# Kernel optimization log

Measured on AMD Instinct MI355X. Metric: run time of the kernel, lower is better.

The kernel has to match this reference:

```python
import jax, jax.numpy as jnp
import numpy as np

N1, N2, N3, N4, D = 50000, 100000, 200000, 300000, 256


def setup_inputs() -> dict:
    key = jax.random.key(0)
    ks = jax.random.split(key, 10)
    feat = jax.random.normal(ks[0], (N1, D), dtype=jnp.float32) * 0.5  # scaled so level-4 products stay bounded
    c2a = jax.random.randint(ks[1], (N2,), 0, N1)
    c2b = jax.random.randint(ks[2], (N2,), 0, N1)
    c3a = jax.random.randint(ks[3], (N3,), 0, N2)
    c3b = jax.random.randint(ks[4], (N3,), 0, N2)
    c4a = jax.random.randint(ks[5], (N4,), 0, N3)
    c4b = jax.random.randint(ks[6], (N4,), 0, N3)
    W = jax.random.normal(ks[7], (D, D), dtype=jnp.float32) / jnp.sqrt(jnp.float32(D))
    b = jax.random.normal(ks[8], (D,), dtype=jnp.float32) * 0.01
    return {"feat": feat, "c2a": c2a, "c2b": c2b, "c3a": c3a, "c3b": c3b,
            "c4a": c4a, "c4b": c4b, "W": W, "b": b}


def _scatter_sum(h_parent, ca, cb, num_children):
    # each parent sends its feature to both children; children sum incoming messages
    z = jnp.zeros((num_children, h_parent.shape[1]), dtype=h_parent.dtype)
    return z.at[ca].add(h_parent).at[cb].add(h_parent)


def reference(feat, c2a, c2b, c3a, c3b, c4a, c4b, W, b):
    # upward: prod reduction over the two constituent subpaths (mailbox prod, dim=1)
    h1 = feat
    h2 = h1[c2a] * h1[c2b]            # [N2, D]
    h3 = h2[c3a] * h2[c3b]            # [N3, D]
    h4 = h3[c4a] * h3[c4b]            # [N4, D]
    # downward: sum-scatter parent -> children, h = h + h_down
    h3 = h3 + _scatter_sum(h4, c4a, c4b, h3.shape[0])
    h2 = h2 + _scatter_sum(h3, c3a, c3b, h2.shape[0])
    h1 = h1 + _scatter_sum(h2, c2a, c2b, h1.shape[0])
    # apply_nodes on n1: Linear + SiLU
    out = jax.nn.silu(h1 @ W + b)
    return out
```

## Files before the change

kernel.cpp:

```cpp
#include <hip/hip_runtime.h>
#include <cstdint>
#include <cstddef>

#define DD 256
#define SCAN_BLK 256
#define SCAN_ELEMS 2048

__device__ __forceinline__ float4 ldrow(const float* __restrict__ base, int row, int lane) {
    return ((const float4*)(base + (size_t)row * DD))[lane];
}
__device__ __forceinline__ float4 mul4(float4 a, float4 b) {
    return make_float4(a.x * b.x, a.y * b.y, a.z * b.z, a.w * b.w);
}
__device__ __forceinline__ float4 add4(float4 a, float4 b) {
    return make_float4(a.x + b.x, a.y + b.y, a.z + b.z, a.w + b.w);
}

__global__ void k_count_pairs(const int* __restrict__ ea, const int* __restrict__ eb,
                              int ne, int* __restrict__ cnt) {
    int e = blockIdx.x * blockDim.x + threadIdx.x;
    if (e >= ne) return;
    atomicAdd(&cnt[ea[e]], 1);
    atomicAdd(&cnt[eb[e]], 1);
}

__global__ void k_fill_edges(const int* __restrict__ ea, const int* __restrict__ eb,
                             int ne, int* __restrict__ cursor, int* __restrict__ ent) {
    int e = blockIdx.x * blockDim.x + threadIdx.x;
    if (e >= ne) return;
    int a = ea[e], b = eb[e];
    int pa = atomicAdd(&cursor[a], 1);
    int pb = atomicAdd(&cursor[b], 1);
    ent[pa] = e;
    ent[pb] = e;
}

__global__ void k_fill_pairs4(const int* __restrict__ c4a, const int* __restrict__ c4b,
                              const int* __restrict__ c3a, const int* __restrict__ c3b,
                              int ne, int* __restrict__ cursor, int2* __restrict__ entp) {
    int e = blockIdx.x * blockDim.x + threadIdx.x;
    if (e >= ne) return;
    int a = c4a[e], b = c4b[e];
    int2 prA = make_int2(c3a[b], c3b[b]);
    int2 prB = make_int2(c3a[a], c3b[a]);
    int pa = atomicAdd(&cursor[a], 1);
    int pb = atomicAdd(&cursor[b], 1);
    entp[pa] = prA;
    entp[pb] = prB;
}

__global__ void k_block_sums(const int* __restrict__ cnt, int n, int* __restrict__ bsum) {
    __shared__ int sdata[SCAN_BLK];
    int base = blockIdx.x * SCAN_ELEMS;
    int s = 0;
#pragma unroll
    for (int k = 0; k < 8; ++k) {
        int idx = base + threadIdx.x + k * SCAN_BLK;
        if (idx < n) s += cnt[idx];
    }
    sdata[threadIdx.x] = s;
    __syncthreads();
    for (int off = SCAN_BLK / 2; off > 0; off >>= 1) {
        if (threadIdx.x < off) sdata[threadIdx.x] += sdata[threadIdx.x + off];
        __syncthreads();
    }
    if (threadIdx.x == 0) bsum[blockIdx.x] = sdata[0];
}

__global__ void k_scan_bsums(int* __restrict__ bsum, int nb, int* __restrict__ total_out) {
    if (threadIdx.x == 0 && blockIdx.x == 0) {
        int acc = 0;
        for (int b = 0; b < nb; ++b) { int v = bsum[b]; bsum[b] = acc; acc += v; }
        *total_out = acc;
    }
}

__global__ void k_scan_final(const int* __restrict__ cnt, int n,
                             const int* __restrict__ bsum, int* __restrict__ offs) {
    __shared__ int sdata[SCAN_BLK];
    int base = blockIdx.x * SCAN_ELEMS;
    int t0 = base + threadIdx.x * 8;
    int loc[8];
    int s = 0;
#pragma unroll
    for (int k = 0; k < 8; ++k) {
        int idx = t0 + k;
        int v = (idx < n) ? cnt[idx] : 0;
        loc[k] = s;
        s += v;
    }
    sdata[threadIdx.x] = s;
    __syncthreads();
    int run = s;
    for (int off = 1; off < SCAN_BLK; off <<= 1) {
        int add = (threadIdx.x >= (unsigned)off) ? sdata[threadIdx.x - off] : 0;
        __syncthreads();
        run += add;
        sdata[threadIdx.x] = run;
        __syncthreads();
    }
    int texcl = run - s + bsum[blockIdx.x];
#pragma unroll
    for (int k = 0; k < 8; ++k) {
        int idx = t0 + k;
        if (idx < n) offs[idx] = texcl + loc[k];
    }
}

__global__ void k_flat_cnt(const int* __restrict__ offs2, const int* __restrict__ ent2,
                           const int* __restrict__ offs3, int n1, int* __restrict__ cntF) {
    int i = blockIdx.x * blockDim.x + threadIdx.x;
    if (i >= n1) return;
    int c = 0;
    int e0 = offs2[i], e1 = offs2[i + 1];
    for (int e = e0; e < e1; ++e) {
        int q = ent2[e];
        c += offs3[q + 1] - offs3[q];
    }
    cntF[i] = c;
}

__global__ void k_flat_fill(const int* __restrict__ offs2, const int* __restrict__ ent2,
                            const int* __restrict__ offs3, const int* __restrict__ ent3,
                            const int* __restrict__ offsF, int n1, int* __restrict__ entF) {
    int i = blockIdx.x * blockDim.x + threadIdx.x;
    if (i >= n1) return;
    int pos = offsF[i];
    int e0 = offs2[i], e1 = offs2[i + 1];
    for (int e = e0; e < e1; ++e) {
        int q = ent2[e];
        int f0 = offs3[q], f1 = offs3[q + 1];
        for (int f = f0; f < f1; ++f) entF[pos++] = ent3[f];
    }
}

__global__ void k_h2(const float* __restrict__ feat, const int* __restrict__ c2a,
                     const int* __restrict__ c2b, float* __restrict__ h2, int n2) {
    int q = blockIdx.x * 4 + (threadIdx.x >> 6);
    int lane = threadIdx.x & 63;
    if (q >= n2) return;
    float4 v = mul4(ldrow(feat, c2a[q], lane), ldrow(feat, c2b[q], lane));
    ((float4*)(h2 + (size_t)q * DD))[lane] = v;
}

__global__ void k_out_init(const float* __restrict__ feat, const float* __restrict__ h2,
                           const int* __restrict__ offs2, const int* __restrict__ ent2,
                           float* __restrict__ out, int n1) {
    int i = blockIdx.x * 4 + (threadIdx.x >> 6);
    int lane = threadIdx.x & 63;
    if (i >= n1) return;
    float4 h = ldrow(feat, i, lane);
    int e0 = offs2[i], e1 = offs2[i + 1];
    int e = e0;
    for (; e + 1 < e1; e += 2) {
        int q0 = ent2[e], q1 = ent2[e + 1];
        float4 v0 = ldrow(h2, q0, lane), v1 = ldrow(h2, q1, lane);
        h = add4(h, add4(v0, v1));
    }
    if (e < e1) h = add4(h, ldrow(h2, ent2[e], lane));
    ((float4*)(out + (size_t)i * DD))[lane] = h;
}

__global__ void k_h3tot_h2(const float* __restrict__ h2,
                           const int* __restrict__ c3a, const int* __restrict__ c3b,
                           const int* __restrict__ offs4, const int2* __restrict__ entp,
                           float* __restrict__ h3chunk, int lo, int hi) {
    int j = lo + blockIdx.x * 4 + (threadIdx.x >> 6);
    int lane = threadIdx.x & 63;
    if (j >= hi) return;
    float4 own = mul4(ldrow(h2, c3a[j], lane), ldrow(h2, c3b[j], lane));
    float4 s = make_float4(0.f, 0.f, 0.f, 0.f);
    int e0 = offs4[j], e1 = offs4[j + 1];
    int e = e0;
    for (; e + 1 < e1; e += 2) {
        int2 p0 = entp[e], p1 = entp[e + 1];
        float4 a0 = ldrow(h2, p0.x, lane), b0 = ldrow(h2, p0.y, lane);
        float4 a1 = ldrow(h2, p1.x, lane), b1 = ldrow(h2, p1.y, lane);
        s = add4(s, add4(mul4(a0, b0), mul4(a1, b1)));
    }
    if (e < e1) {
        int2 p = entp[e];
        s = add4(s, mul4(ldrow(h2, p.x, lane), ldrow(h2, p.y, lane)));
    }
    float4 r = mul4(own, make_float4(1.f + s.x, 1.f + s.y, 1.f + s.z, 1.f + s.w));
    ((float4*)(h3chunk + (size_t)(j - lo) * DD))[lane] = r;
}

__global__ void k_h1_flat(const int* __restrict__ offsF, const int* __restrict__ entF,
                          const float* __restrict__ h3chunk,
                          float* __restrict__ out, int n1, int lo, int hi) {
    int i = blockIdx.x * 4 + (threadIdx.x >> 6);
    int lane = threadIdx.x & 63;
    if (i >= n1) return;
    float4 h = ldrow(out, i, lane);
    int f0 = offsF[i], f1 = offsF[i + 1];
    int f = f0;
    for (; f + 1 < f1; f += 2) {
        int j0 = entF[f], j1 = entF[f + 1];
        bool in0 = (j0 >= lo) && (j0 < hi);
        bool in1 = (j1 >= lo) && (j1 < hi);
        if (in0 && in1) {
            float4 v0 = ldrow(h3chunk, j0 - lo, lane);
            float4 v1 = ldrow(h3chunk, j1 - lo, lane);
            h = add4(h, add4(v0, v1));
        } else if (in0) {
            h = add4(h, ldrow(h3chunk, j0 - lo, lane));
        } else if (in1) {
            h = add4(h, ldrow(h3chunk, j1 - lo, lane));
        }
    }
    if (f < f1) {
        int j0 = entF[f];
        if (j0 >= lo && j0 < hi) h = add4(h, ldrow(h3chunk, j0 - lo, lane));
    }
    ((float4*)(out + (size_t)i * DD))[lane] = h;
}

__device__ __forceinline__ float silu_f(float x) { return x / (1.0f + expf(-x)); }

__global__ __launch_bounds__(256) void k_gemm_silu(float* __restrict__ h,
                                                   const float* __restrict__ W,
                                                   const float* __restrict__ bias,
                                                   int n1) {
    __shared__ float As[32 * DD];
    const int t = threadIdx.x;
    const int row0 = blockIdx.x * 32;

    const float4* hv = (const float4*)h;
    float4* As4 = (float4*)As;
#pragma unroll
    for (int i = 0; i < 8; ++i) {
        int idx = t + i * 256;
        int r = idx >> 6, c = idx & 63;
        int gr = row0 + r;
        float4 v = make_float4(0.f, 0.f, 0.f, 0.f);
        if (gr < n1) v = hv[(size_t)gr * 64 + c];
        As4[idx] = v;
    }
    __syncthreads();

    const int rg = t >> 6;
    const int cg = t & 63;
    const float4* Wv = (const float4*)W;

    float4 acc[8];
#pragma unroll
    for (int r = 0; r < 8; ++r) acc[r] = make_float4(0.f, 0.f, 0.f, 0.f);

    for (int k = 0; k < DD; k += 4) {
        float4 a[8];
#pragma unroll
        for (int r = 0; r < 8; ++r)
            a[r] = *(const float4*)&As[(rg * 8 + r) * DD + k];
#pragma unroll
        for (int kk = 0; kk < 4; ++kk) {
            float4 w = Wv[(size_t)(k + kk) * 64 + cg];
#pragma unroll
            for (int r = 0; r < 8; ++r) {
                float av = (kk == 0) ? a[r].x : (kk == 1) ? a[r].y
                         : (kk == 2) ? a[r].z : a[r].w;
                acc[r].x += av * w.x;
                acc[r].y += av * w.y;
                acc[r].z += av * w.z;
                acc[r].w += av * w.w;
            }
        }
    }

    float4 bb = ((const float4*)bias)[cg];
    float4* ho = (float4*)h;
#pragma unroll
    for (int r = 0; r < 8; ++r) {
        int gr = row0 + rg * 8 + r;
        if (gr >= n1) continue;
        float4 x = acc[r];
        x.x = silu_f(x.x + bb.x);
        x.y = silu_f(x.y + bb.y);
        x.z = silu_f(x.z + bb.z);
        x.w = silu_f(x.w + bb.w);
        ho[(size_t)gr * 64 + cg] = x;
    }
}

static inline size_t al16(size_t x) { return (x + 15) & ~(size_t)15; }

extern "C" void kernel_launch(void* const* d_in, const int* in_sizes, int n_in,
                              void* d_out, int out_size, void* d_ws, size_t ws_size,
                              hipStream_t stream) {
    const float* feat = (const float*)d_in[0];
    const int* c2a = (const int*)d_in[1];
    const int* c2b = (const int*)d_in[2];
    const int* c3a = (const int*)d_in[3];
    const int* c3b = (const int*)d_in[4];
    const int* c4a = (const int*)d_in[5];
    const int* c4b = (const int*)d_in[6];
    const float* W = (const float*)d_in[7];
    const float* bias = (const float*)d_in[8];

    const int N1 = in_sizes[0] / DD;
    const int N2 = in_sizes[1];
    const int N3 = in_sizes[3];
    const int N4 = in_sizes[5];
    float* out = (float*)d_out;
    char* ws = (char*)d_ws;

    dim3 blk(256);
    auto rows_grid = [](int n) { return dim3((unsigned)((n + 3) / 4)); };
    auto thr_grid = [](int n) { return dim3((unsigned)((n + 255) / 256)); };

    int maxN = N1 > N2 ? N1 : N2;
    if (N3 > maxN) maxN = N3;

    size_t cnt_b   = al16((size_t)maxN * 4);
    size_t bsum_b  = al16(4096);
    size_t offs4_b = al16((size_t)(N3 + 1) * 4);
    size_t entp_b  = al16((size_t)2 * N4 * 8);
    size_t offs3_b = al16((size_t)(N2 + 1) * 4);
    size_t ent3_b  = al16((size_t)2 * N3 * 4);
    size_t offs2_b = al16((size_t)(N1 + 1) * 4);
    size_t ent2_b  = al16((size_t)2 * N2 * 4);
    size_t offsF_b = al16((size_t)(N1 + 1) * 4);
    size_t entF_b  = al16((size_t)4 * N3 * 4);
    size_t fixed_b = cnt_b + bsum_b + offs4_b + entp_b + offs3_b + ent3_b +
                     offs2_b + ent2_b + offsF_b + entF_b;
    size_t h2_b = (size_t)N2 * DD * sizeof(float);

    char* p = ws;
    int* cnt   = (int*)p; p += cnt_b;
    int* bsum  = (int*)p; p += bsum_b;
    int* offs4 = (int*)p; p += offs4_b;
    int2* entp = (int2*)p; p += entp_b;
    int* offs3 = (int*)p; p += offs3_b;
    int* ent3  = (int*)p; p += ent3_b;
    int* offs2 = (int*)p; p += offs2_b;
    int* ent2  = (int*)p; p += ent2_b;
    int* offsF = (int*)p; p += offsF_b;
    int* entF  = (int*)p; p += entF_b;
    float* h2  = (float*)p; p += h2_b;
    float* h3chunk = (float*)p;

    size_t free_b = (ws_size > fixed_b + h2_b) ? ws_size - fixed_b - h2_b : 0;
    int chunk_rows = (int)(free_b / ((size_t)DD * sizeof(float)));
    if (chunk_rows > N3) chunk_rows = N3;
    if (chunk_rows < 1) chunk_rows = 1;
    int C = (N3 + chunk_rows - 1) / chunk_rows;
    chunk_rows = (N3 + C - 1) / C;

    auto scan_offs = [&](int* cn, int nnode, int* offs) {
        int nb = (nnode + SCAN_ELEMS - 1) / SCAN_ELEMS;
        k_block_sums<<<dim3((unsigned)nb), dim3(SCAN_BLK), 0, stream>>>(cn, nnode, bsum);
        k_scan_bsums<<<dim3(1), dim3(64), 0, stream>>>(bsum, nb, offs + nnode);
        k_scan_final<<<dim3((unsigned)nb), dim3(SCAN_BLK), 0, stream>>>(cn, nnode, bsum, offs);
    };

    hipMemsetAsync(cnt, 0, (size_t)N3 * 4, stream);
    k_count_pairs<<<thr_grid(N4), blk, 0, stream>>>(c4a, c4b, N4, cnt);
    scan_offs(cnt, N3, offs4);
    hipMemcpyAsync(cnt, offs4, (size_t)N3 * 4, hipMemcpyDeviceToDevice, stream);
    k_fill_pairs4<<<thr_grid(N4), blk, 0, stream>>>(c4a, c4b, c3a, c3b, N4, cnt, entp);

    hipMemsetAsync(cnt, 0, (size_t)N2 * 4, stream);
    k_count_pairs<<<thr_grid(N3), blk, 0, stream>>>(c3a, c3b, N3, cnt);
    scan_offs(cnt, N2, offs3);
    hipMemcpyAsync(cnt, offs3, (size_t)N2 * 4, hipMemcpyDeviceToDevice, stream);
    k_fill_edges<<<thr_grid(N3), blk, 0, stream>>>(c3a, c3b, N3, cnt, ent3);

    hipMemsetAsync(cnt, 0, (size_t)N1 * 4, stream);
    k_count_pairs<<<thr_grid(N2), blk, 0, stream>>>(c2a, c2b, N2, cnt);
    scan_offs(cnt, N1, offs2);
    hipMemcpyAsync(cnt, offs2, (size_t)N1 * 4, hipMemcpyDeviceToDevice, stream);
    k_fill_edges<<<thr_grid(N2), blk, 0, stream>>>(c2a, c2b, N2, cnt, ent2);

    k_flat_cnt<<<thr_grid(N1), blk, 0, stream>>>(offs2, ent2, offs3, N1, cnt);
    scan_offs(cnt, N1, offsF);
    k_flat_fill<<<thr_grid(N1), blk, 0, stream>>>(offs2, ent2, offs3, ent3, offsF, N1, entF);

    k_h2<<<rows_grid(N2), blk, 0, stream>>>(feat, c2a, c2b, h2, N2);
    k_out_init<<<rows_grid(N1), blk, 0, stream>>>(feat, h2, offs2, ent2, out, N1);

    for (int lo = 0; lo < N3; lo += chunk_rows) {
        int hi = lo + chunk_rows;
        if (hi > N3) hi = N3;
        k_h3tot_h2<<<rows_grid(hi - lo), blk, 0, stream>>>(h2, c3a, c3b, offs4, entp,
                                                           h3chunk, lo, hi);
        k_h1_flat<<<rows_grid(N1), blk, 0, stream>>>(offsF, entF, h3chunk, out, N1, lo, hi);
    }

    k_gemm_silu<<<dim3((unsigned)((N1 + 31) / 32)), blk, 0, stream>>>(out, W, bias, N1);
}
```

Baseline: 857.0 us.

## Split feature dimension into two halves to shrink gather working set

The h2/h3 pipeline now runs twice, once per 128-column half of the feature dimension, using half-width h2 and h3 buffers and float2 loads. Each half of h2 (about 51 MB) is more likely to sit in the large last-level cache during the random-gather k_h3tot pass, and the h3 chunk can hold twice as many rows, so fewer chunks are needed. The separate out-init kernel is folded into the first h1 pass of each half. In exchange there are twice as many kernel launches, index arrays are re-read per half, and the float2 accesses are narrower per lane.

```diff
diff --git a/kernel.cpp b/kernel.cpp
--- a/kernel.cpp
+++ b/kernel.cpp
@@ -3,17 +3,21 @@
 #include <cstddef>
 
 #define DD 256
+#define DH 128
 #define SCAN_BLK 256
 #define SCAN_ELEMS 2048
 
-__device__ __forceinline__ float4 ldrow(const float* __restrict__ base, int row, int lane) {
-    return ((const float4*)(base + (size_t)row * DD))[lane];
-}
-__device__ __forceinline__ float4 mul4(float4 a, float4 b) {
-    return make_float4(a.x * b.x, a.y * b.y, a.z * b.z, a.w * b.w);
-}
-__device__ __forceinline__ float4 add4(float4 a, float4 b) {
-    return make_float4(a.x + b.x, a.y + b.y, a.z + b.z, a.w + b.w);
+__device__ __forceinline__ float2 mul2(float2 a, float2 b) {
+    return make_float2(a.x * b.x, a.y * b.y);
+}
+__device__ __forceinline__ float2 add2(float2 a, float2 b) {
+    return make_float2(a.x + b.x, a.y + b.y);
+}
+__device__ __forceinline__ float2 ldh(const float* __restrict__ base, int row, int lane) {
+    return ((const float2*)(base + (size_t)row * DH))[lane];
+}
+__device__ __forceinline__ float2 ldf(const float* __restrict__ base, int row, int doff, int lane) {
+    return ((const float2*)(base + (size_t)row * DD + doff))[lane];
 }
 
 __global__ void k_count_pairs(const int* __restrict__ ea, const int* __restrict__ eb,
@@ -134,65 +138,62 @@
     }
 }
 
-__global__ void k_h2(const float* __restrict__ feat, const int* __restrict__ c2a,
-                     const int* __restrict__ c2b, float* __restrict__ h2, int n2) {
+__global__ void k_h2_half(const float* __restrict__ feat, const int* __restrict__ c2a,
+                          const int* __restrict__ c2b, float* __restrict__ h2h,
+                          int n2, int doff) {
     int q = blockIdx.x * 4 + (threadIdx.x >> 6);
     int lane = threadIdx.x & 63;
     if (q >= n2) return;
-    float4 v = mul4(ldrow(feat, c2a[q], lane), ldrow(feat, c2b[q], lane));
-    ((float4*)(h2 + (size_t)q * DD))[lane] = v;
-}
-
-__global__ void k_out_init(const float* __restrict__ feat, const float* __restrict__ h2,
-                           const int* __restrict__ offs2, const int* __restrict__ ent2,
-                           float* __restrict__ out, int n1) {
-    int i = blockIdx.x * 4 + (threadIdx.x >> 6);
-    int lane = threadIdx.x & 63;
-    if (i >= n1) return;
-    float4 h = ldrow(feat, i, lane);
-    int e0 = offs2[i], e1 = offs2[i + 1];
-    int e = e0;
-    for (; e + 1 < e1; e += 2) {
-        int q0 = ent2[e], q1 = ent2[e + 1];
-        float4 v0 = ldrow(h2, q0, lane), v1 = ldrow(h2, q1, lane);
-        h = add4(h, add4(v0, v1));
-    }
-    if (e < e1) h = add4(h, ldrow(h2, ent2[e], lane));
-    ((float4*)(out + (size_t)i * DD))[lane] = h;
-}
-
-__global__ void k_h3tot_h2(const float* __restrict__ h2,
-                           const int* __restrict__ c3a, const int* __restrict__ c3b,
-                           const int* __restrict__ offs4, const int2* __restrict__ entp,
-                           float* __restrict__ h3chunk, int lo, int hi) {
+    float2 v = mul2(ldf(feat, c2a[q], doff, lane), ldf(feat, c2b[q], doff, lane));
+    ((float2*)(h2h + (size_t)q * DH))[lane] = v;
+}
+
+__global__ void k_h3tot_half(const float* __restrict__ h2h,
+                             const int* __restrict__ c3a, const int* __restrict__ c3b,
+                             const int* __restrict__ offs4, const int2* __restrict__ entp,
+                             float* __restrict__ h3th, int lo, int hi) {
     int j = lo + blockIdx.x * 4 + (threadIdx.x >> 6);
     int lane = threadIdx.x & 63;
     if (j >= hi) return;
-    float4 own = mul4(ldrow(h2, c3a[j], lane), ldrow(h2, c3b[j], lane));
-    float4 s = make_float4(0.f, 0.f, 0.f, 0.f);
+    float2 own = mul2(ldh(h2h, c3a[j], lane), ldh(h2h, c3b[j], lane));
+    float2 s = make_float2(0.f, 0.f);
     int e0 = offs4[j], e1 = offs4[j + 1];
     int e = e0;
     for (; e + 1 < e1; e += 2) {
         int2 p0 = entp[e], p1 = entp[e + 1];
-        float4 a0 = ldrow(h2, p0.x, lane), b0 = ldrow(h2, p0.y, lane);
-        float4 a1 = ldrow(h2, p1.x, lane), b1 = ldrow(h2, p1.y, lane);
-        s = add4(s, add4(mul4(a0, b0), mul4(a1, b1)));
+        float2 a0 = ldh(h2h, p0.x, lane), b0 = ldh(h2h, p0.y, lane);
+        float2 a1 = ldh(h2h, p1.x, lane), b1 = ldh(h2h, p1.y, lane);
+        s = add2(s, add2(mul2(a0, b0), mul2(a1, b1)));
     }
     if (e < e1) {
         int2 p = entp[e];
-        s = add4(s, mul4(ldrow(h2, p.x, lane), ldrow(h2, p.y, lane)));
-    }
-    float4 r = mul4(own, make_float4(1.f + s.x, 1.f + s.y, 1.f + s.z, 1.f + s.w));
-    ((float4*)(h3chunk + (size_t)(j - lo) * DD))[lane] = r;
-}
-
-__global__ void k_h1_flat(const int* __restrict__ offsF, const int* __restrict__ entF,
-                          const float* __restrict__ h3chunk,
-                          float* __restrict__ out, int n1, int lo, int hi) {
+        s = add2(s, mul2(ldh(h2h, p.x, lane), ldh(h2h, p.y, lane)));
+    }
+    float2 r = mul2(own, make_float2(1.f + s.x, 1.f + s.y));
+    ((float2*)(h3th + (size_t)(j - lo) * DH))[lane] = r;
+}
+
+__global__ void k_h1_half(const float* __restrict__ feat, const float* __restrict__ h2h,
+                          const int* __restrict__ offs2, const int* __restrict__ ent2,
+                          const int* __restrict__ offsF, const int* __restrict__ entF,
+                          const float* __restrict__ h3th, float* __restrict__ out,
+                          int n1, int lo, int hi, int do_init, int doff) {
     int i = blockIdx.x * 4 + (threadIdx.x >> 6);
     int lane = threadIdx.x & 63;
     if (i >= n1) return;
-    float4 h = ldrow(out, i, lane);
+    float2 h;
+    if (do_init) {
+        h = ldf(feat, i, doff, lane);
+        int e0 = offs2[i], e1 = offs2[i + 1];
+        int e = e0;
+        for (; e + 1 < e1; e += 2) {
+            int q0 = ent2[e], q1 = ent2[e + 1];
+            h = add2(h, add2(ldh(h2h, q0, lane), ldh(h2h, q1, lane)));
+        }
+        if (e < e1) h = add2(h, ldh(h2h, ent2[e], lane));
+    } else {
+        h = ldf(out, i, doff, lane);
+    }
     int f0 = offsF[i], f1 = offsF[i + 1];
     int f = f0;
     for (; f + 1 < f1; f += 2) {
@@ -200,20 +201,18 @@
         bool in0 = (j0 >= lo) && (j0 < hi);
         bool in1 = (j1 >= lo) && (j1 < hi);
         if (in0 && in1) {
-            float4 v0 = ldrow(h3chunk, j0 - lo, lane);
-            float4 v1 = ldrow(h3chunk, j1 - lo, lane);
-            h = add4(h, add4(v0, v1));
+            h = add2(h, add2(ldh(h3th, j0 - lo, lane), ldh(h3th, j1 - lo, lane)));
         } else if (in0) {
-            h = add4(h, ldrow(h3chunk, j0 - lo, lane));
+            h = add2(h, ldh(h3th, j0 - lo, lane));
         } else if (in1) {
-            h = add4(h, ldrow(h3chunk, j1 - lo, lane));
+            h = add2(h, ldh(h3th, j1 - lo, lane));
         }
     }
     if (f < f1) {
         int j0 = entF[f];
-        if (j0 >= lo && j0 < hi) h = add4(h, ldrow(h3chunk, j0 - lo, lane));
-    }
-    ((float4*)(out + (size_t)i * DD))[lane] = h;
+        if (j0 >= lo && j0 < hi) h = add2(h, ldh(h3th, j0 - lo, lane));
+    }
+    ((float2*)(out + (size_t)i * DD + doff))[lane] = h;
 }
 
 __device__ __forceinline__ float silu_f(float x) { return x / (1.0f + expf(-x)); }
@@ -323,7 +322,7 @@
     size_t entF_b  = al16((size_t)4 * N3 * 4);
     size_t fixed_b = cnt_b + bsum_b + offs4_b + entp_b + offs3_b + ent3_b +
                      offs2_b + ent2_b + offsF_b + entF_b;
-    size_t h2_b = (size_t)N2 * DD * sizeof(float);
+    size_t h2h_b = (size_t)N2 * DH * sizeof(float);
 
     char* p = ws;
     int* cnt   = (int*)p; p += cnt_b;
@@ -336,11 +335,11 @@
     int* ent2  = (int*)p; p += ent2_b;
     int* offsF = (int*)p; p += offsF_b;
     int* entF  = (int*)p; p += entF_b;
-    float* h2  = (float*)p; p += h2_b;
-    float* h3chunk = (float*)p;
-
-    size_t free_b = (ws_size > fixed_b + h2_b) ? ws_size - fixed_b - h2_b : 0;
-    int chunk_rows = (int)(free_b / ((size_t)DD * sizeof(float)));
+    float* h2h = (float*)p; p += h2h_b;
+    float* h3th = (float*)p;
+
+    size_t free_b = (ws_size > fixed_b + h2h_b) ? ws_size - fixed_b - h2h_b : 0;
+    int chunk_rows = (int)(free_b / ((size_t)DH * sizeof(float)));
     if (chunk_rows > N3) chunk_rows = N3;
     if (chunk_rows < 1) chunk_rows = 1;
     int C = (N3 + chunk_rows - 1) / chunk_rows;
@@ -375,15 +374,20 @@
     scan_offs(cnt, N1, offsF);
     k_flat_fill<<<thr_grid(N1), blk, 0, stream>>>(offs2, ent2, offs3, ent3, offsF, N1, entF);
 
-    k_h2<<<rows_grid(N2), blk, 0, stream>>>(feat, c2a, c2b, h2, N2);
-    k_out_init<<<rows_grid(N1), blk, 0, stream>>>(feat, h2, offs2, ent2, out, N1);
-
-    for (int lo = 0; lo < N3; lo += chunk_rows) {
-        int hi = lo + chunk_rows;
-        if (hi > N3) hi = N3;
-        k_h3tot_h2<<<rows_grid(hi - lo), blk, 0, stream>>>(h2, c3a, c3b, offs4, entp,
-                                                           h3chunk, lo, hi);
-        k_h1_flat<<<rows_grid(N1), blk, 0, stream>>>(offsF, entF, h3chunk, out, N1, lo, hi);
+    for (int doff = 0; doff < DD; doff += DH) {
+        k_h2_half<<<rows_grid(N2), blk, 0, stream>>>(feat, c2a, c2b, h2h, N2, doff);
+        int do_init = 1;
+        for (int lo = 0; lo < N3; lo += chunk_rows) {
+            int hi = lo + chunk_rows;
+            if (hi > N3) hi = N3;
+            k_h3tot_half<<<rows_grid(hi - lo), blk, 0, stream>>>(h2h, c3a, c3b,
+                                                                 offs4, entp,
+                                                                 h3th, lo, hi);
+            k_h1_half<<<rows_grid(N1), blk, 0, stream>>>(feat, h2h, offs2, ent2,
+                                                         offsF, entF, h3th, out,
+                                                         N1, lo, hi, do_init, doff);
+            do_init = 0;
+        }
     }
 
     k_gemm_silu<<<dim3((unsigned)((N1 + 31) / 32)), blk, 0, stream>>>(out, W, bias, N1);
```

New measurement: 852.8 us. Within noise of the previous version (-0.5%).
